# Kernel tuning notes

Measured on AMD Instinct MI355X. Metric: run time of the kernel, lower is better.

Reference implementation:

```python
import jax, jax.numpy as jnp
import numpy as np

N_NODES = 100000
N_EDGES = 1600000
DIM = 32  # size_in


def setup_inputs() -> dict:
    key = jax.random.key(0)
    k = jax.random.split(key, 8)
    N, E, D = N_NODES, N_EDGES, DIM
    x = jax.random.normal(k[0], (N, 2 * D), dtype=jnp.float32)
    edge_index = jax.random.randint(k[1], (2, E), 0, N, dtype=jnp.int64)
    # Glorot-ish scaled weights (PyG GCNConv uses glorot init); biases zero.
    W1 = jax.random.normal(k[2], (2 * D, 2 * D), dtype=jnp.float32) * (1.0 / np.sqrt(2 * D))
    b1 = jnp.zeros((2 * D,), dtype=jnp.float32)
    W2 = jax.random.normal(k[3], (2 * D, D), dtype=jnp.float32) * (1.0 / np.sqrt(2 * D))
    b2 = jnp.zeros((D,), dtype=jnp.float32)
    W3 = jax.random.normal(k[4], (D, 1), dtype=jnp.float32) * (1.0 / np.sqrt(D))
    b3 = jnp.zeros((1,), dtype=jnp.float32)
    return {"x": x, "edge_index": edge_index, "W1": W1, "b1": b1,
            "W2": W2, "b2": b2, "W3": W3, "b3": b3}


def _gcn_norm(edge_index, num_nodes):
    # PyG gcn_norm with add_self_loops=True, edge_weight=1:
    # deg[i] = # incoming edges (incl. self loop); norm_e = deg[src]^-1/2 * deg[dst]^-1/2
    loop = jnp.arange(num_nodes, dtype=edge_index.dtype)
    src = jnp.concatenate([edge_index[0], loop])
    dst = jnp.concatenate([edge_index[1], loop])
    ones = jnp.ones(src.shape[0], dtype=jnp.float32)
    deg = jax.ops.segment_sum(ones, dst, num_segments=num_nodes)
    dis = jnp.where(deg > 0, jax.lax.rsqrt(deg), 0.0)
    norm = dis[src] * dis[dst]
    return src, dst, norm


def _gcn_conv(h, W, b, src, dst, norm, num_nodes):
    # linear transform first (PyG order), then normalized scatter-add aggregation
    h = h @ W  # [N, out]
    msg = h[src] * norm[:, None]  # gather over edges
    agg = jax.ops.segment_sum(msg, dst, num_segments=num_nodes)
    return agg + b


def reference(x, edge_index, W1, b1, W2, b2, W3, b3):
    N = x.shape[0]
    src, dst, norm = _gcn_norm(edge_index, N)
    out = jnp.tanh(_gcn_conv(x, W1, b1, src, dst, norm, N))
    out = jnp.tanh(_gcn_conv(out, W2, b2, src, dst, norm, N))
    out = _gcn_conv(out, W3, b3, src, dst, norm, N)
    return out
```

## Files before the change

### kernel.cpp

```cpp
#include <hip/hip_runtime.h>
#include <hip/hip_fp16.h>
#include <math.h>

static constexpr int NN = 100000;
static constexpr int NE = 1600000;
static constexpr int BUCK_SH = 5;
static constexpr int NBUK = NN >> BUCK_SH;
static constexpr int NCH = 256;
static constexpr int CH = NE / NCH;

__global__ __launch_bounds__(256)
void k_chist(const int* __restrict__ ei, int* __restrict__ H) {
  __shared__ int h[NBUK];
  for (int i = threadIdx.x; i < NBUK; i += 256) h[i] = 0;
  __syncthreads();
  int chunk = blockIdx.x;
  int start = chunk * CH;
  for (int e = start + threadIdx.x; e < start + CH; e += 256)
    atomicAdd(&h[ei[NE + e] >> BUCK_SH], 1);
  __syncthreads();
  int* Hc = H + chunk * NBUK;
  for (int i = threadIdx.x; i < NBUK; i += 256) Hc[i] = h[i];
}

__global__ void k_csum(int* __restrict__ H, int* __restrict__ tot) {
  int b = blockIdx.x * blockDim.x + threadIdx.x;
  if (b >= NBUK) return;
  int acc = 0;
#pragma unroll 4
  for (int c = 0; c < NCH; ++c) {
    int v = H[c * NBUK + b];
    H[c * NBUK + b] = acc;
    acc += v;
  }
  tot[b] = acc;
}

__global__ __launch_bounds__(1024)
void k_bscan(const int* __restrict__ tot, int* __restrict__ boff) {
  __shared__ int buf[1024];
  __shared__ int s_carry;
  int tid = threadIdx.x;
  if (tid == 0) s_carry = 0;
  __syncthreads();
  for (int base = 0; base < NBUK; base += 1024) {
    int i = base + tid;
    int v = (i < NBUK) ? tot[i] : 0;
    buf[tid] = v;
    __syncthreads();
#pragma unroll
    for (int off = 1; off < 1024; off <<= 1) {
      int t = (tid >= off) ? buf[tid - off] : 0;
      __syncthreads();
      buf[tid] += t;
      __syncthreads();
    }
    int excl = buf[tid] - v;
    int carry = s_carry;
    if (i < NBUK) boff[i] = carry + excl;
    __syncthreads();
    if (tid == 1023) s_carry = carry + buf[1023];
    __syncthreads();
  }
  if (tid == 0) boff[NBUK] = s_carry;
}

__global__ __launch_bounds__(1024)
void k_scat(const int* __restrict__ ei, const int* __restrict__ H,
            const int* __restrict__ boff, unsigned* __restrict__ se) {
  __shared__ int cur[NBUK];
  int chunk = blockIdx.x;
  const int* Hc = H + chunk * NBUK;
  for (int i = threadIdx.x; i < NBUK; i += 1024) cur[i] = boff[i] + Hc[i];
  __syncthreads();
  int start = chunk * CH;
  for (int e = start + threadIdx.x; e < start + CH; e += 1024) {
    int src = ei[e], dst = ei[NE + e];
    int pos = atomicAdd(&cur[dst >> BUCK_SH], 1);
    se[pos] = ((unsigned)(dst & 31) << 20) | (unsigned)src;
  }
}

__global__ __launch_bounds__(256)
void k_blocal(const unsigned* __restrict__ se, const int* __restrict__ boff,
              int* __restrict__ rowptr, float* __restrict__ dis, int* __restrict__ csr_src) {
  int b = blockIdx.x;
  int base = boff[b], end = boff[b + 1];
  __shared__ int cnt[32], off[32];
  int tid = threadIdx.x;
  if (tid < 32) cnt[tid] = 0;
  __syncthreads();
  for (int k = base + tid; k < end; k += 256)
    atomicAdd(&cnt[se[k] >> 20], 1);
  __syncthreads();
  if (tid == 0) {
    int acc = 0;
#pragma unroll
    for (int i = 0; i < 32; ++i) { off[i] = acc; acc += cnt[i]; }
  }
  __syncthreads();
  if (tid < 32) {
    int node = (b << BUCK_SH) + tid;
    rowptr[node] = base + off[tid];
    dis[node] = rsqrtf(1.0f + (float)cnt[tid]);
    cnt[tid] = 0;
  }
  if (b == 0 && tid == 64) rowptr[NN] = NE;
  __syncthreads();
  for (int k = base + tid; k < end; k += 256) {
    unsigned e = se[k];
    int dl = e >> 20;
    int pos = base + off[dl] + atomicAdd(&cnt[dl], 1);
    csr_src[pos] = (int)(e & 0xFFFFFu);
  }
}

__global__ __launch_bounds__(256)
void k_gemm64_h(const float* __restrict__ in, const float* __restrict__ W,
                const float* __restrict__ dis, __half* __restrict__ g) {
  __shared__ float rows[16 * 64];
  int c = threadIdx.x & 63;
  int wid = threadIdx.x >> 6;
  float Wc[64];
#pragma unroll
  for (int k = 0; k < 64; ++k) Wc[k] = W[k * 64 + c];
  int tiles = NN / 16;
  for (int t = blockIdx.x; t < tiles; t += gridDim.x) {
    int row0 = t * 16;
    __syncthreads();
    ((float4*)rows)[threadIdx.x] = ((const float4*)(in + (size_t)row0 * 64))[threadIdx.x];
    __syncthreads();
#pragma unroll
    for (int r = 0; r < 4; ++r) {
      const float* rp = rows + (wid * 4 + r) * 64;
      float acc = 0.f;
#pragma unroll
      for (int kc = 0; kc < 64; kc += 4) {
        float4 v = *(const float4*)(rp + kc);
        acc = fmaf(v.x, Wc[kc + 0], acc);
        acc = fmaf(v.y, Wc[kc + 1], acc);
        acc = fmaf(v.z, Wc[kc + 2], acc);
        acc = fmaf(v.w, Wc[kc + 3], acc);
      }
      int row = row0 + wid * 4 + r;
      g[row * 64 + c] = __float2half(acc * dis[row]);
    }
  }
}

__global__ __launch_bounds__(256)
void k_gemm32_h(const __half* __restrict__ inh, const float* __restrict__ W,
                const float* __restrict__ dis, __half* __restrict__ g) {
  __shared__ float rows[16 * 64];
  int lane = threadIdx.x & 63;
  int c = lane & 31;
  int ksub = lane >> 5;
  int wid = threadIdx.x >> 6;
  float Wc[32];
#pragma unroll
  for (int k = 0; k < 32; ++k) Wc[k] = W[(ksub * 32 + k) * 32 + c];
  int tiles = NN / 16;
  for (int t = blockIdx.x; t < tiles; t += gridDim.x) {
    int row0 = t * 16;
    __syncthreads();
    {
      float2 raw = ((const float2*)(inh + (size_t)row0 * 64))[threadIdx.x];
      __half2* hp = (__half2*)&raw;
      float2 f01 = __half22float2(hp[0]);
      float2 f23 = __half22float2(hp[1]);
      float4 w = {f01.x, f01.y, f23.x, f23.y};
      ((float4*)rows)[threadIdx.x] = w;
    }
    __syncthreads();
#pragma unroll
    for (int r = 0; r < 4; ++r) {
      const float* rp = rows + (wid * 4 + r) * 64 + ksub * 32;
      float acc = 0.f;
#pragma unroll
      for (int kc = 0; kc < 32; kc += 4) {
        float4 v = *(const float4*)(rp + kc);
        acc = fmaf(v.x, Wc[kc + 0], acc);
        acc = fmaf(v.y, Wc[kc + 1], acc);
        acc = fmaf(v.z, Wc[kc + 2], acc);
        acc = fmaf(v.w, Wc[kc + 3], acc);
      }
      acc += __shfl_down(acc, 32);
      int row = row0 + wid * 4 + r;
      if (ksub == 0) g[row * 32 + c] = __float2half(acc * dis[row]);
    }
  }
}

__device__ __forceinline__ float fast_tanh(float x) {
  float e = __expf(2.0f * x);
  return 1.0f - 2.0f / (e + 1.0f);
}

__device__ __forceinline__ void upadd8(float4 r, float4& lo, float4& hi) {
  __half2* h = (__half2*)&r;
  float2 f0 = __half22float2(h[0]);
  float2 f1 = __half22float2(h[1]);
  float2 f2 = __half22float2(h[2]);
  float2 f3 = __half22float2(h[3]);
  lo.x += f0.x; lo.y += f0.y; lo.z += f1.x; lo.w += f1.y;
  hi.x += f2.x; hi.y += f2.y; hi.z += f3.x; hi.w += f3.y;
}

__global__ __launch_bounds__(256)
void k_agg64v(const int* __restrict__ rowptr, const int* __restrict__ csr_src,
              const __half* __restrict__ g, const float* __restrict__ dis,
              const float* __restrict__ b, __half* __restrict__ outh) {
  int lane = threadIdx.x & 63;
  int grp = lane >> 3;
  int cl = lane & 7;
  int node = blockIdx.x * 32 + (threadIdx.x >> 6) * 8 + grp;
  if (node >= NN) return;
  const char* base = (const char*)g;
  float4 l0 = {0,0,0,0}, h0 = {0,0,0,0}, l1 = {0,0,0,0}, h1 = {0,0,0,0};
  float4 l2 = {0,0,0,0}, h2 = {0,0,0,0}, l3 = {0,0,0,0}, h3 = {0,0,0,0};
  {
    float4 r = *(const float4*)(base + (size_t)node * 128 + cl * 16);
    upadd8(r, l0, h0);
  }
  int k = rowptr[node], end = rowptr[node + 1];
  for (; k + 4 <= end; k += 4) {
    int s0 = csr_src[k], s1 = csr_src[k + 1], s2 = csr_src[k + 2], s3 = csr_src[k + 3];
    float4 r0 = *(const float4*)(base + (size_t)s0 * 128 + cl * 16);
    float4 r1 = *(const float4*)(base + (size_t)s1 * 128 + cl * 16);
    float4 r2 = *(const float4*)(base + (size_t)s2 * 128 + cl * 16);
    float4 r3 = *(const float4*)(base + (size_t)s3 * 128 + cl * 16);
    upadd8(r0, l0, h0); upadd8(r1, l1, h1);
    upadd8(r2, l2, h2); upadd8(r3, l3, h3);
  }
  for (; k < end; ++k) {
    float4 r = *(const float4*)(base + (size_t)csr_src[k] * 128 + cl * 16);
    upadd8(r, l0, h0);
  }
  float d = dis[node];
  float4 blo = *(const float4*)(b + cl * 8);
  float4 bhi = *(const float4*)(b + cl * 8 + 4);
  float4 vl, vh;
  vl.x = ((l0.x + l1.x) + (l2.x + l3.x)) * d + blo.x;
  vl.y = ((l0.y + l1.y) + (l2.y + l3.y)) * d + blo.y;
  vl.z = ((l0.z + l1.z) + (l2.z + l3.z)) * d + blo.z;
  vl.w = ((l0.w + l1.w) + (l2.w + l3.w)) * d + blo.w;
  vh.x = ((h0.x + h1.x) + (h2.x + h3.x)) * d + bhi.x;
  vh.y = ((h0.y + h1.y) + (h2.y + h3.y)) * d + bhi.y;
  vh.z = ((h0.z + h1.z) + (h2.z + h3.z)) * d + bhi.z;
  vh.w = ((h0.w + h1.w) + (h2.w + h3.w)) * d + bhi.w;
  vl.x = fast_tanh(vl.x); vl.y = fast_tanh(vl.y);
  vl.z = fast_tanh(vl.z); vl.w = fast_tanh(vl.w);
  vh.x = fast_tanh(vh.x); vh.y = fast_tanh(vh.y);
  vh.z = fast_tanh(vh.z); vh.w = fast_tanh(vh.w);
  float4 st;
  ((__half2*)&st)[0] = __floats2half2_rn(vl.x, vl.y);
  ((__half2*)&st)[1] = __floats2half2_rn(vl.z, vl.w);
  ((__half2*)&st)[2] = __floats2half2_rn(vh.x, vh.y);
  ((__half2*)&st)[3] = __floats2half2_rn(vh.z, vh.w);
  *(float4*)((char*)outh + (size_t)node * 128 + cl * 16) = st;
}

__global__ __launch_bounds__(256)
void k_agg32v(const int* __restrict__ rowptr, const int* __restrict__ csr_src,
              const __half* __restrict__ g, const float* __restrict__ dis,
              const float* __restrict__ b, const float* __restrict__ W3,
              float* __restrict__ Af) {
  int lane = threadIdx.x & 63;
  int grp = lane >> 3;
  int cl = lane & 7;
  int node = blockIdx.x * 32 + (threadIdx.x >> 6) * 8 + grp;
  if (node >= NN) return;
  const char* base = (const char*)g;
  float4 a0 = {0,0,0,0}, a1 = {0,0,0,0}, a2 = {0,0,0,0}, a3 = {0,0,0,0};
  {
    float2 r = *(const float2*)(base + (size_t)node * 64 + cl * 8);
    __half2* h = (__half2*)&r;
    float2 f0 = __half22float2(h[0]), f1 = __half22float2(h[1]);
    a0.x += f0.x; a0.y += f0.y; a0.z += f1.x; a0.w += f1.y;
  }
  int k = rowptr[node], end = rowptr[node + 1];
  for (; k + 4 <= end; k += 4) {
    int s0 = csr_src[k], s1 = csr_src[k + 1], s2 = csr_src[k + 2], s3 = csr_src[k + 3];
    float2 r0 = *(const float2*)(base + (size_t)s0 * 64 + cl * 8);
    float2 r1 = *(const float2*)(base + (size_t)s1 * 64 + cl * 8);
    float2 r2 = *(const float2*)(base + (size_t)s2 * 64 + cl * 8);
    float2 r3 = *(const float2*)(base + (size_t)s3 * 64 + cl * 8);
    __half2* h0 = (__half2*)&r0; __half2* h1 = (__half2*)&r1;
    __half2* h2 = (__half2*)&r2; __half2* h3 = (__half2*)&r3;
    float2 f;
    f = __half22float2(h0[0]); a0.x += f.x; a0.y += f.y;
    f = __half22float2(h0[1]); a0.z += f.x; a0.w += f.y;
    f = __half22float2(h1[0]); a1.x += f.x; a1.y += f.y;
    f = __half22float2(h1[1]); a1.z += f.x; a1.w += f.y;
    f = __half22float2(h2[0]); a2.x += f.x; a2.y += f.y;
    f = __half22float2(h2[1]); a2.z += f.x; a2.w += f.y;
    f = __half22float2(h3[0]); a3.x += f.x; a3.y += f.y;
    f = __half22float2(h3[1]); a3.z += f.x; a3.w += f.y;
  }
  for (; k < end; ++k) {
    float2 r = *(const float2*)(base + (size_t)csr_src[k] * 64 + cl * 8);
    __half2* h = (__half2*)&r;
    float2 f0 = __half22float2(h[0]), f1 = __half22float2(h[1]);
    a0.x += f0.x; a0.y += f0.y; a0.z += f1.x; a0.w += f1.y;
  }
  float d = dis[node];
  float4 bb = *(const float4*)(b + cl * 4);
  float4 v;
  v.x = ((a0.x + a1.x) + (a2.x + a3.x)) * d + bb.x;
  v.y = ((a0.y + a1.y) + (a2.y + a3.y)) * d + bb.y;
  v.z = ((a0.z + a1.z) + (a2.z + a3.z)) * d + bb.z;
  v.w = ((a0.w + a1.w) + (a2.w + a3.w)) * d + bb.w;
  v.x = fast_tanh(v.x); v.y = fast_tanh(v.y);
  v.z = fast_tanh(v.z); v.w = fast_tanh(v.w);
  float4 w3 = *(const float4*)(W3 + cl * 4);
  float p = v.x * w3.x + v.y * w3.y + v.z * w3.z + v.w * w3.w;
  p += __shfl_xor(p, 1);
  p += __shfl_xor(p, 2);
  p += __shfl_xor(p, 4);
  if (cl == 0) Af[node] = p * d;
}

__global__ void k_agg1(const int* __restrict__ rowptr, const int* __restrict__ csr_src,
                       const float* __restrict__ g, const float* __restrict__ dis,
                       const float* __restrict__ b, float* __restrict__ out) {
  int node = blockIdx.x * blockDim.x + threadIdx.x;
  if (node >= NN) return;
  float a0 = g[node], a1 = 0.f, a2 = 0.f, a3 = 0.f;
  int beg = rowptr[node], end = rowptr[node + 1];
  int k = beg;
  for (; k + 4 <= end; k += 4) {
    float m0 = g[csr_src[k]], m1 = g[csr_src[k + 1]];
    float m2 = g[csr_src[k + 2]], m3 = g[csr_src[k + 3]];
    a0 += m0; a1 += m1; a2 += m2; a3 += m3;
  }
  for (; k < end; ++k) a0 += g[csr_src[k]];
  out[node] = ((a0 + a1) + (a2 + a3)) * dis[node] + b[0];
}

extern "C" void kernel_launch(void* const* d_in, const int* in_sizes, int n_in,
                              void* d_out, int out_size, void* d_ws, size_t ws_size,
                              hipStream_t stream) {
  const float* x  = (const float*)d_in[0];
  const int*   ei = (const int*)d_in[1];
  const float* W1 = (const float*)d_in[2];
  const float* b1 = (const float*)d_in[3];
  const float* W2 = (const float*)d_in[4];
  const float* b2 = (const float*)d_in[5];
  const float* W3 = (const float*)d_in[6];
  const float* b3 = (const float*)d_in[7];
  float* out = (float*)d_out;

  char* ws = (char*)d_ws;
  int*      H       = (int*)ws;      ws += (size_t)NCH * NBUK * 4;
  int*      tot     = (int*)ws;      ws += ((NBUK + 255)/256)*256 * 4;
  int*      boff    = (int*)ws;      ws += ((NBUK + 1 + 255)/256)*256 * 4;
  unsigned* se      = (unsigned*)ws; ws += (size_t)NE * 4;
  int*      rowptr  = (int*)ws;      ws += ((NN + 1 + 255)/256)*256 * 4;
  int*      csr_src = (int*)ws;      ws += (size_t)NE * 4;
  float*    dis     = (float*)ws;    ws += ((NN + 255)/256)*256 * 4;
  __half*   Ah      = (__half*)ws;   ws += (size_t)NN * 64 * 2;
  __half*   B1h     = (__half*)ws;   ws += (size_t)NN * 64 * 2;
  float*    Af      = (float*)ws;    ws += (size_t)NN * 4;

  k_chist <<<NCH, 256, 0, stream>>>(ei, H);
  k_csum  <<<(NBUK + 255) / 256, 256, 0, stream>>>(H, tot);
  k_bscan <<<1, 1024, 0, stream>>>(tot, boff);
  k_scat  <<<NCH, 1024, 0, stream>>>(ei, H, boff, se);
  k_blocal<<<NBUK, 256, 0, stream>>>(se, boff, rowptr, dis, csr_src);

  k_gemm64_h<<<1250, 256, 0, stream>>>(x, W1, dis, Ah);
  k_agg64v<<<(NN + 31) / 32, 256, 0, stream>>>(rowptr, csr_src, Ah, dis, b1, B1h);

  k_gemm32_h<<<1250, 256, 0, stream>>>(B1h, W2, dis, Ah);
  k_agg32v<<<(NN + 31) / 32, 256, 0, stream>>>(rowptr, csr_src, Ah, dis, b2, W3, Af);

  k_agg1<<<(NN + 255) / 256, 256, 0, stream>>>(rowptr, csr_src, Af, dis, b3, out);
}
```

Before: 260.5 us.

## Fuse layer-2 GEMM into layer-1 aggregation epilogue and unroll agg32 by 8

The layer-1 aggregation kernel now stages its tanh outputs for 32 nodes in shared memory and applies the W2 projection in place, scaled by dis, writing the 32-wide half-precision features straight out. This removes the separate k_gemm32_h launch and the write and re-read of the 64-wide intermediate buffer. The layer-2 aggregation gather loop is also unrolled to 8 edges for more memory-level parallelism. The trade-off is higher register use in the fused kernel (32 W values held per thread plus the accumulators) and an added block-wide barrier. The node bounds check was dropped, which relies on NN being a multiple of 32.

```diff
diff --git a/kernel.cpp b/kernel.cpp
--- a/kernel.cpp
+++ b/kernel.cpp
@@ -148,49 +148,6 @@
   }
 }
 
-__global__ __launch_bounds__(256)
-void k_gemm32_h(const __half* __restrict__ inh, const float* __restrict__ W,
-                const float* __restrict__ dis, __half* __restrict__ g) {
-  __shared__ float rows[16 * 64];
-  int lane = threadIdx.x & 63;
-  int c = lane & 31;
-  int ksub = lane >> 5;
-  int wid = threadIdx.x >> 6;
-  float Wc[32];
-#pragma unroll
-  for (int k = 0; k < 32; ++k) Wc[k] = W[(ksub * 32 + k) * 32 + c];
-  int tiles = NN / 16;
-  for (int t = blockIdx.x; t < tiles; t += gridDim.x) {
-    int row0 = t * 16;
-    __syncthreads();
-    {
-      float2 raw = ((const float2*)(inh + (size_t)row0 * 64))[threadIdx.x];
-      __half2* hp = (__half2*)&raw;
-      float2 f01 = __half22float2(hp[0]);
-      float2 f23 = __half22float2(hp[1]);
-      float4 w = {f01.x, f01.y, f23.x, f23.y};
-      ((float4*)rows)[threadIdx.x] = w;
-    }
-    __syncthreads();
-#pragma unroll
-    for (int r = 0; r < 4; ++r) {
-      const float* rp = rows + (wid * 4 + r) * 64 + ksub * 32;
-      float acc = 0.f;
-#pragma unroll
-      for (int kc = 0; kc < 32; kc += 4) {
-        float4 v = *(const float4*)(rp + kc);
-        acc = fmaf(v.x, Wc[kc + 0], acc);
-        acc = fmaf(v.y, Wc[kc + 1], acc);
-        acc = fmaf(v.z, Wc[kc + 2], acc);
-        acc = fmaf(v.w, Wc[kc + 3], acc);
-      }
-      acc += __shfl_down(acc, 32);
-      int row = row0 + wid * 4 + r;
-      if (ksub == 0) g[row * 32 + c] = __float2half(acc * dis[row]);
-    }
-  }
-}
-
 __device__ __forceinline__ float fast_tanh(float x) {
   float e = __expf(2.0f * x);
   return 1.0f - 2.0f / (e + 1.0f);
@@ -207,14 +164,23 @@
 }
 
 __global__ __launch_bounds__(256)
-void k_agg64v(const int* __restrict__ rowptr, const int* __restrict__ csr_src,
+void k_agg64f(const int* __restrict__ rowptr, const int* __restrict__ csr_src,
               const __half* __restrict__ g, const float* __restrict__ dis,
-              const float* __restrict__ b, __half* __restrict__ outh) {
+              const float* __restrict__ b, const float* __restrict__ W2,
+              __half* __restrict__ g2) {
+  __shared__ float tile[4][8][64];
   int lane = threadIdx.x & 63;
+  int wid = threadIdx.x >> 6;
   int grp = lane >> 3;
   int cl = lane & 7;
-  int node = blockIdx.x * 32 + (threadIdx.x >> 6) * 8 + grp;
-  if (node >= NN) return;
+  int node = blockIdx.x * 32 + wid * 8 + grp;
+
+  int c2 = lane & 31;
+  int ksub = lane >> 5;
+  float Wc[32];
+#pragma unroll
+  for (int k = 0; k < 32; ++k) Wc[k] = W2[(ksub * 32 + k) * 32 + c2];
+
   const char* base = (const char*)g;
   float4 l0 = {0,0,0,0}, h0 = {0,0,0,0}, l1 = {0,0,0,0}, h1 = {0,0,0,0};
   float4 l2 = {0,0,0,0}, h2 = {0,0,0,0}, l3 = {0,0,0,0}, h3 = {0,0,0,0};
@@ -252,12 +218,28 @@
   vl.z = fast_tanh(vl.z); vl.w = fast_tanh(vl.w);
   vh.x = fast_tanh(vh.x); vh.y = fast_tanh(vh.y);
   vh.z = fast_tanh(vh.z); vh.w = fast_tanh(vh.w);
-  float4 st;
-  ((__half2*)&st)[0] = __floats2half2_rn(vl.x, vl.y);
-  ((__half2*)&st)[1] = __floats2half2_rn(vl.z, vl.w);
-  ((__half2*)&st)[2] = __floats2half2_rn(vh.x, vh.y);
-  ((__half2*)&st)[3] = __floats2half2_rn(vh.z, vh.w);
-  *(float4*)((char*)outh + (size_t)node * 128 + cl * 16) = st;
+
+  *(float4*)&tile[wid][grp][cl * 8] = vl;
+  *(float4*)&tile[wid][grp][cl * 8 + 4] = vh;
+  __syncthreads();
+
+  int rbase = blockIdx.x * 32 + wid * 8;
+#pragma unroll
+  for (int r = 0; r < 8; ++r) {
+    const float* rp = &tile[wid][r][ksub * 32];
+    float acc = 0.f;
+#pragma unroll
+    for (int kc = 0; kc < 32; kc += 4) {
+      float4 v = *(const float4*)(rp + kc);
+      acc = fmaf(v.x, Wc[kc + 0], acc);
+      acc = fmaf(v.y, Wc[kc + 1], acc);
+      acc = fmaf(v.z, Wc[kc + 2], acc);
+      acc = fmaf(v.w, Wc[kc + 3], acc);
+    }
+    acc += __shfl_down(acc, 32);
+    int row = rbase + r;
+    if (ksub == 0) g2[row * 32 + c2] = __float2half(acc * dis[row]);
+  }
 }
 
 __global__ __launch_bounds__(256)
@@ -279,23 +261,47 @@
     a0.x += f0.x; a0.y += f0.y; a0.z += f1.x; a0.w += f1.y;
   }
   int k = rowptr[node], end = rowptr[node + 1];
+  for (; k + 8 <= end; k += 8) {
+    float2 r0 = *(const float2*)(base + (size_t)csr_src[k + 0] * 64 + cl * 8);
+    float2 r1 = *(const float2*)(base + (size_t)csr_src[k + 1] * 64 + cl * 8);
+    float2 r2 = *(const float2*)(base + (size_t)csr_src[k + 2] * 64 + cl * 8);
+    float2 r3 = *(const float2*)(base + (size_t)csr_src[k + 3] * 64 + cl * 8);
+    float2 r4 = *(const float2*)(base + (size_t)csr_src[k + 4] * 64 + cl * 8);
+    float2 r5 = *(const float2*)(base + (size_t)csr_src[k + 5] * 64 + cl * 8);
+    float2 r6 = *(const float2*)(base + (size_t)csr_src[k + 6] * 64 + cl * 8);
+    float2 r7 = *(const float2*)(base + (size_t)csr_src[k + 7] * 64 + cl * 8);
+    __half2* h; float2 f;
+    h = (__half2*)&r0; f = __half22float2(h[0]); a0.x += f.x; a0.y += f.y;
+    f = __half22float2(h[1]); a0.z += f.x; a0.w += f.y;
+    h = (__half2*)&r1; f = __half22float2(h[0]); a1.x += f.x; a1.y += f.y;
+    f = __half22float2(h[1]); a1.z += f.x; a1.w += f.y;
+    h = (__half2*)&r2; f = __half22float2(h[0]); a2.x += f.x; a2.y += f.y;
+    f = __half22float2(h[1]); a2.z += f.x; a2.w += f.y;
+    h = (__half2*)&r3; f = __half22float2(h[0]); a3.x += f.x; a3.y += f.y;
+    f = __half22float2(h[1]); a3.z += f.x; a3.w += f.y;
+    h = (__half2*)&r4; f = __half22float2(h[0]); a0.x += f.x; a0.y += f.y;
+    f = __half22float2(h[1]); a0.z += f.x; a0.w += f.y;
+    h = (__half2*)&r5; f = __half22float2(h[0]); a1.x += f.x; a1.y += f.y;
+    f = __half22float2(h[1]); a1.z += f.x; a1.w += f.y;
+    h = (__half2*)&r6; f = __half22float2(h[0]); a2.x += f.x; a2.y += f.y;
+    f = __half22float2(h[1]); a2.z += f.x; a2.w += f.y;
+    h = (__half2*)&r7; f = __half22float2(h[0]); a3.x += f.x; a3.y += f.y;
+    f = __half22float2(h[1]); a3.z += f.x; a3.w += f.y;
+  }
   for (; k + 4 <= end; k += 4) {
-    int s0 = csr_src[k], s1 = csr_src[k + 1], s2 = csr_src[k + 2], s3 = csr_src[k + 3];
-    float2 r0 = *(const float2*)(base + (size_t)s0 * 64 + cl * 8);
-    float2 r1 = *(const float2*)(base + (size_t)s1 * 64 + cl * 8);
-    float2 r2 = *(const float2*)(base + (size_t)s2 * 64 + cl * 8);
-    float2 r3 = *(const float2*)(base + (size_t)s3 * 64 + cl * 8);
-    __half2* h0 = (__half2*)&r0; __half2* h1 = (__half2*)&r1;
-    __half2* h2 = (__half2*)&r2; __half2* h3 = (__half2*)&r3;
-    float2 f;
-    f = __half22float2(h0[0]); a0.x += f.x; a0.y += f.y;
-    f = __half22float2(h0[1]); a0.z += f.x; a0.w += f.y;
-    f = __half22float2(h1[0]); a1.x += f.x; a1.y += f.y;
-    f = __half22float2(h1[1]); a1.z += f.x; a1.w += f.y;
-    f = __half22float2(h2[0]); a2.x += f.x; a2.y += f.y;
-    f = __half22float2(h2[1]); a2.z += f.x; a2.w += f.y;
-    f = __half22float2(h3[0]); a3.x += f.x; a3.y += f.y;
-    f = __half22float2(h3[1]); a3.z += f.x; a3.w += f.y;
+    float2 r0 = *(const float2*)(base + (size_t)csr_src[k + 0] * 64 + cl * 8);
+    float2 r1 = *(const float2*)(base + (size_t)csr_src[k + 1] * 64 + cl * 8);
+    float2 r2 = *(const float2*)(base + (size_t)csr_src[k + 2] * 64 + cl * 8);
+    float2 r3 = *(const float2*)(base + (size_t)csr_src[k + 3] * 64 + cl * 8);
+    __half2* h; float2 f;
+    h = (__half2*)&r0; f = __half22float2(h[0]); a0.x += f.x; a0.y += f.y;
+    f = __half22float2(h[1]); a0.z += f.x; a0.w += f.y;
+    h = (__half2*)&r1; f = __half22float2(h[0]); a1.x += f.x; a1.y += f.y;
+    f = __half22float2(h[1]); a1.z += f.x; a1.w += f.y;
+    h = (__half2*)&r2; f = __half22float2(h[0]); a2.x += f.x; a2.y += f.y;
+    f = __half22float2(h[1]); a2.z += f.x; a2.w += f.y;
+    h = (__half2*)&r3; f = __half22float2(h[0]); a3.x += f.x; a3.y += f.y;
+    f = __half22float2(h[1]); a3.z += f.x; a3.w += f.y;
   }
   for (; k < end; ++k) {
     float2 r = *(const float2*)(base + (size_t)csr_src[k] * 64 + cl * 8);
@@ -359,7 +365,7 @@
   int*      csr_src = (int*)ws;      ws += (size_t)NE * 4;
   float*    dis     = (float*)ws;    ws += ((NN + 255)/256)*256 * 4;
   __half*   Ah      = (__half*)ws;   ws += (size_t)NN * 64 * 2;
-  __half*   B1h     = (__half*)ws;   ws += (size_t)NN * 64 * 2;
+  __half*   Ah2     = (__half*)ws;   ws += (size_t)NN * 32 * 2;
   float*    Af      = (float*)ws;    ws += (size_t)NN * 4;
 
   k_chist <<<NCH, 256, 0, stream>>>(ei, H);
@@ -369,10 +375,7 @@
   k_blocal<<<NBUK, 256, 0, stream>>>(se, boff, rowptr, dis, csr_src);
 
   k_gemm64_h<<<1250, 256, 0, stream>>>(x, W1, dis, Ah);
-  k_agg64v<<<(NN + 31) / 32, 256, 0, stream>>>(rowptr, csr_src, Ah, dis, b1, B1h);
-
-  k_gemm32_h<<<1250, 256, 0, stream>>>(B1h, W2, dis, Ah);
-  k_agg32v<<<(NN + 31) / 32, 256, 0, stream>>>(rowptr, csr_src, Ah, dis, b2, W3, Af);
-
+  k_agg64f<<<NN / 32, 256, 0, stream>>>(rowptr, csr_src, Ah, dis, b1, W2, Ah2);
+  k_agg32v<<<NN / 32, 256, 0, stream>>>(rowptr, csr_src, Ah2, dis, b2, W3, Af);
   k_agg1<<<(NN + 255) / 256, 256, 0, stream>>>(rowptr, csr_src, Af, dis, b3, out);
 }
```

After: 251.7 us. -3.4%, faster.
